# Optimization experiments

Measured on AMD Instinct MI355X. Metric: run time of the kernel, lower is better.

## Reference

```python
import jax, jax.numpy as jnp
import numpy as np

HEAD_DIM = 128

def setup_inputs() -> dict:
    key = jax.random.key(0)
    k1, k2, k3 = jax.random.split(key, 3)
    B, S, H, Hkv, D = 2, 2048, 32, 8, HEAD_DIM
    q = jax.random.normal(k1, (B, S, H, D), dtype=jnp.float32)
    k = jax.random.normal(k2, (B, S, Hkv, D), dtype=jnp.float32)
    v = jax.random.normal(k3, (B, S, Hkv, D), dtype=jnp.float32)
    return {"q": q, "k": k, "v": v}

def reference(q, k, v):
    # Causal GQA attention, same math as SDPA(is_causal=True, scale=head_dim**-0.5)
    # q: [B,S,H,D], k/v: [B,S,Hkv,D]; H = Hkv * G (grouped-query attention)
    B, S, H, D = q.shape
    Hkv = k.shape[2]
    G = H // Hkv
    scale = jnp.asarray(D, q.dtype) ** -0.5
    qg = q.reshape(B, S, Hkv, G, D)
    # scores: [B, Hkv, G, Sq, Sk]
    scores = jnp.einsum('bqhgd,bkhd->bhgqk', qg, k) * scale
    causal = jnp.tril(jnp.ones((S, S), dtype=bool))  # [Sq, Sk]
    scores = jnp.where(causal, scores, jnp.asarray(-jnp.inf, scores.dtype))
    probs = jax.nn.softmax(scores, axis=-1)
    out = jnp.einsum('bhgqk,bkhd->bqhgd', probs, v)
    return out.reshape(B, S, H, D)
```

## Files before the change

### kernel.cpp

```cpp
#include <hip/hip_runtime.h>
#include <hip/hip_bf16.h>

typedef short bf16x8 __attribute__((ext_vector_type(8)));
typedef float f32x4  __attribute__((ext_vector_type(4)));

#define B_    2
#define S_    2048
#define H_    32
#define HKV_  8
#define D_    128
#define QBLK  64
#define QBLK2 128
#define KVB   32
#define SCALE 0.1275431741f

static __device__ inline float exp2_fast(float x) {
    return __builtin_amdgcn_exp2f(x);
}

static __device__ inline unsigned short f2bf(float f) {
    unsigned u = __builtin_bit_cast(unsigned, f);
    u += 0x7fffu + ((u >> 16) & 1u);
    return (unsigned short)(u >> 16);
}
static __device__ inline unsigned pk2(float a, float b) {
    return (unsigned)f2bf(a) | ((unsigned)f2bf(b) << 16);
}
static __device__ inline short cvt_bf(float f) {
    __hip_bfloat16 h = __float2bfloat16(f);
    return __builtin_bit_cast(short, h);
}
static __device__ inline void gload16(const unsigned char* g, unsigned char* l) {
    __builtin_amdgcn_global_load_lds(
        (const __attribute__((address_space(1))) void*)g,
        (__attribute__((address_space(3))) void*)l, 16, 0, 0);
}

__global__ __launch_bounds__(256) void prep_k(const float* __restrict__ Kg,
                                              unsigned char* __restrict__ Kb) {
    const int s   = blockIdx.x * 256 + threadIdx.x;
    const int seg = s & 15;
    const int kv  = (s >> 4) & (S_ - 1);
    const int bhk = s >> 15;
    const int hk  = bhk & (HKV_ - 1);
    const int b   = bhk >> 3;
    const float* src = Kg + ((size_t)(b * S_ + kv) * HKV_ + hk) * D_ + seg * 8;
    float4 x0 = *(const float4*)(src);
    float4 x1 = *(const float4*)(src + 4);
    uint4 u = { pk2(x0.x, x0.y), pk2(x0.z, x0.w), pk2(x1.x, x1.y), pk2(x1.z, x1.w) };
    *(uint4*)(Kb + ((size_t)(b * HKV_ + hk) * S_ + kv) * 256 + ((seg * 16) ^ ((kv & 7) << 4))) = u;
}

__global__ __launch_bounds__(256) void prep_v(const float* __restrict__ Vg,
                                              unsigned short* __restrict__ Vb) {
    const int blk  = blockIdx.x;
    const int half = blk & 1;
    const int tile = (blk >> 1) & 63;
    const int hk   = (blk >> 7) & (HKV_ - 1);
    const int b    = blk >> 10;
    const int t    = threadIdx.x;
    const int kp0  = (t & 3) * 8;
    const int d    = (t >> 2) + half * 64;
    const int kv0  = tile * KVB;
    unsigned short tmp[8];
#pragma unroll
    for (int j = 0; j < 8; ++j) {
        const int kp = kp0 + j;
        const int kv = (((kp >> 2) & 1) << 4) + ((kp >> 3) << 2) + (kp & 3);
        tmp[j] = f2bf(Vg[((size_t)(b * S_ + kv0 + kv) * HKV_ + hk) * D_ + d]);
    }
    unsigned short* dst = Vb + ((size_t)(b * HKV_ + hk) * 64 + tile) * (128 * 32) + d * 32 + kp0;
    *(uint4*)dst = *(uint4*)tmp;
}

__global__ __launch_bounds__(256) void fattn2(
        const float* __restrict__ Qg, const unsigned char* __restrict__ Kb,
        const unsigned char* __restrict__ Vb, float* __restrict__ Og) {
    __shared__ __align__(16) unsigned char lds[2 * 16384];

    const int tid  = threadIdx.x;
    const int lane = tid & 63;
    const int w    = tid >> 6;
    const int m    = lane & 15;
    const int g    = lane >> 4;
    const int lane16 = lane * 16;

    const int SQ  = S_ / QBLK2;
    const int bid = blockIdx.x;
    const int qt  = (SQ - 1) - (bid >> 6);
    const int hb  = bid & 63;
    const int h   = hb & (H_ - 1);
    const int b   = hb >> 5;
    const int hk  = h >> 2;

    const int qB    = qt * QBLK2;
    const int q0w   = qB + w * 32;
    const int qA    = q0w + m;
    const int qgate = q0w + 31;

    const unsigned char* KbH = Kb + (size_t)(b * HKV_ + hk) * S_ * 256;
    const unsigned char* VbH = Vb + (size_t)(b * HKV_ + hk) * 64 * 8192;

    bf16x8 qfA[4], qfB[4];
    {
        const float* qrowA = Qg + (size_t)((b * S_ + qA) * H_ + h) * D_;
        const float* qrowB = qrowA + (size_t)16 * H_ * D_;
#pragma unroll
        for (int db = 0; db < 4; ++db) {
            const float* pA = qrowA + db * 32 + g * 8;
            const float* pB = qrowB + db * 32 + g * 8;
            float4 a0 = *(const float4*)(pA);
            float4 a1 = *(const float4*)(pA + 4);
            float4 b0 = *(const float4*)(pB);
            float4 b1 = *(const float4*)(pB + 4);
            bf16x8 qa, qb;
            qa[0] = cvt_bf(a0.x * SCALE); qa[1] = cvt_bf(a0.y * SCALE);
            qa[2] = cvt_bf(a0.z * SCALE); qa[3] = cvt_bf(a0.w * SCALE);
            qa[4] = cvt_bf(a1.x * SCALE); qa[5] = cvt_bf(a1.y * SCALE);
            qa[6] = cvt_bf(a1.z * SCALE); qa[7] = cvt_bf(a1.w * SCALE);
            qb[0] = cvt_bf(b0.x * SCALE); qb[1] = cvt_bf(b0.y * SCALE);
            qb[2] = cvt_bf(b0.z * SCALE); qb[3] = cvt_bf(b0.w * SCALE);
            qb[4] = cvt_bf(b1.x * SCALE); qb[5] = cvt_bf(b1.y * SCALE);
            qb[6] = cvt_bf(b1.z * SCALE); qb[7] = cvt_bf(b1.w * SCALE);
            qfA[db] = qa; qfB[db] = qb;
        }
    }

    f32x4 oaccA[8], oaccB[8];
#pragma unroll
    for (int i = 0; i < 8; ++i) {
        oaccA[i] = (f32x4){0.f, 0.f, 0.f, 0.f};
        oaccB[i] = (f32x4){0.f, 0.f, 0.f, 0.f};
    }
    float m_run = 4.0f, lsumA = 0.f, lsumB = 0.f;

#define STAGE(kt, cbuf) do {                                                  \
        const unsigned char* KbT = KbH + (size_t)(kt) * (KVB * 256);          \
        const unsigned char* VbT = VbH + (size_t)(kt) * 8192;                 \
        unsigned char* dK = lds + (cbuf) * 16384;                             \
        unsigned char* dV = dK + 8192;                                        \
        gload16(KbT + (w * 2 + 0) * 1024 + lane16, dK + (w * 2 + 0) * 1024);  \
        gload16(KbT + (w * 2 + 1) * 1024 + lane16, dK + (w * 2 + 1) * 1024);  \
        gload16(VbT + (w * 2 + 0) * 1024 + lane16, dV + (w * 2 + 0) * 1024);  \
        gload16(VbT + (w * 2 + 1) * 1024 + lane16, dV + (w * 2 + 1) * 1024);  \
    } while (0)

    const int nt = (qB + QBLK2) / KVB;
    int cur = 0;
    STAGE(0, 0);
    asm volatile("s_waitcnt vmcnt(0)" ::: "memory");
    __builtin_amdgcn_s_barrier();

    for (int t = 0; t < nt; ++t) {
        const int kv0 = t * KVB;
        if (t + 1 < nt) STAGE(t + 1, cur ^ 1);

        if (kv0 <= qgate) {
            const unsigned char* cK = lds + cur * 16384;
            const unsigned char* cV = cK + 8192;

            const f32x4 cinit = (f32x4){-m_run, -m_run, -m_run, -m_run};
            f32x4 stA0 = cinit, stA1 = cinit, stB0 = cinit, stB1 = cinit;
            const int sw = (m & 7) << 4;
            __builtin_amdgcn_s_setprio(1);
#pragma unroll
            for (int db = 0; db < 4; ++db) {
                bf16x8 kf0 = *(const bf16x8*)(cK + (m     ) * 256 + ((db * 64 + g * 16) ^ sw));
                bf16x8 kf1 = *(const bf16x8*)(cK + (m + 16) * 256 + ((db * 64 + g * 16) ^ sw));
                stA0 = __builtin_amdgcn_mfma_f32_16x16x32_bf16(kf0, qfA[db], stA0, 0, 0, 0);
                stA1 = __builtin_amdgcn_mfma_f32_16x16x32_bf16(kf1, qfA[db], stA1, 0, 0, 0);
                stB0 = __builtin_amdgcn_mfma_f32_16x16x32_bf16(kf0, qfB[db], stB0, 0, 0, 0);
                stB1 = __builtin_amdgcn_mfma_f32_16x16x32_bf16(kf1, qfB[db], stB1, 0, 0, 0);
            }
            __builtin_amdgcn_s_setprio(0);

            if (kv0 + (KVB - 1) > q0w) {
                const int qBrow = qA + 16;
#pragma unroll
                for (int jj = 0; jj < 4; ++jj) {
                    const int kva = kv0 + g * 4 + jj;
                    if (kva      > qA)    stA0[jj] = -1e30f;
                    if (kva + 16 > qA)    stA1[jj] = -1e30f;
                    if (kva      > qBrow) stB0[jj] = -1e30f;
                    if (kva + 16 > qBrow) stB1[jj] = -1e30f;
                }
            }

            float pmax = -1e30f;
#pragma unroll
            for (int jj = 0; jj < 4; ++jj)
                pmax = fmaxf(pmax, fmaxf(fmaxf(stA0[jj], stA1[jj]),
                                         fmaxf(stB0[jj], stB1[jj])));
            if (__any(pmax > 12.0f)) {
                float dm = fmaxf(pmax, __shfl_xor(pmax, 16));
                dm = fmaxf(dm, __shfl_xor(dm, 32));
                dm = fmaxf(dm, 0.0f);
                const float corr = exp2_fast(-dm);
                lsumA *= corr; lsumB *= corr;
                float cj[4];
#pragma unroll
                for (int jj = 0; jj < 4; ++jj) cj[jj] = __shfl(corr, g * 4 + jj);
#pragma unroll
                for (int i = 0; i < 8; ++i)
#pragma unroll
                    for (int jj = 0; jj < 4; ++jj) {
                        oaccA[i][jj] *= cj[jj];
                        oaccB[i][jj] *= cj[jj];
                    }
                m_run += dm;
#pragma unroll
                for (int jj = 0; jj < 4; ++jj) {
                    stA0[jj] -= dm; stA1[jj] -= dm;
                    stB0[jj] -= dm; stB1[jj] -= dm;
                }
            }

#pragma unroll
            for (int jj = 0; jj < 4; ++jj) {
                stA0[jj] = exp2_fast(stA0[jj]);
                stA1[jj] = exp2_fast(stA1[jj]);
                stB0[jj] = exp2_fast(stB0[jj]);
                stB1[jj] = exp2_fast(stB1[jj]);
            }
            lsumA += ((stA0[0] + stA0[1]) + (stA0[2] + stA0[3]))
                   + ((stA1[0] + stA1[1]) + (stA1[2] + stA1[3]));
            lsumB += ((stB0[0] + stB0[1]) + (stB0[2] + stB0[3]))
                   + ((stB1[0] + stB1[1]) + (stB1[2] + stB1[3]));

            bf16x8 paA, paB;
#pragma unroll
            for (int jj = 0; jj < 4; ++jj) {
                paA[jj]     = cvt_bf(stA0[jj]);
                paA[4 + jj] = cvt_bf(stA1[jj]);
                paB[jj]     = cvt_bf(stB0[jj]);
                paB[4 + jj] = cvt_bf(stB1[jj]);
            }

            __builtin_amdgcn_s_setprio(1);
#pragma unroll
            for (int db8 = 0; db8 < 8; ++db8) {
                bf16x8 vf = *(const bf16x8*)(cV + (db8 * 16 + m) * 64 + g * 16);
                oaccA[db8] = __builtin_amdgcn_mfma_f32_16x16x32_bf16(paA, vf, oaccA[db8], 0, 0, 0);
                oaccB[db8] = __builtin_amdgcn_mfma_f32_16x16x32_bf16(paB, vf, oaccB[db8], 0, 0, 0);
            }
            __builtin_amdgcn_s_setprio(0);
        }

        asm volatile("s_waitcnt vmcnt(0)" ::: "memory");
        __builtin_amdgcn_s_barrier();
        cur ^= 1;
    }
#undef STAGE

    lsumA += __shfl_xor(lsumA, 16); lsumA += __shfl_xor(lsumA, 32);
    lsumB += __shfl_xor(lsumB, 16); lsumB += __shfl_xor(lsumB, 32);
    const float rA = 1.0f / lsumA, rB = 1.0f / lsumB;
    float rsA[4], rsB[4];
#pragma unroll
    for (int jj = 0; jj < 4; ++jj) {
        rsA[jj] = __shfl(rA, g * 4 + jj);
        rsB[jj] = __shfl(rB, g * 4 + jj);
    }
#pragma unroll
    for (int db8 = 0; db8 < 8; ++db8) {
#pragma unroll
        for (int jj = 0; jj < 4; ++jj) {
            const int qrA = q0w + g * 4 + jj;
            Og[(size_t)((b * S_ + qrA) * H_ + h) * D_ + db8 * 16 + m]
                = oaccA[db8][jj] * rsA[jj];
            Og[(size_t)((b * S_ + qrA + 16) * H_ + h) * D_ + db8 * 16 + m]
                = oaccB[db8][jj] * rsB[jj];
        }
    }
}

__global__ __launch_bounds__(256) void fattn_fallback(
        const float* __restrict__ Qg, const float* __restrict__ Kg,
        const float* __restrict__ Vg, float* __restrict__ Og) {
    __shared__ __align__(16) unsigned char  sK[32 * 256];
    __shared__ __align__(16) unsigned short sV[128 * 40];
    const int tid  = threadIdx.x;
    const int lane = tid & 63;
    const int w    = tid >> 6;
    const int m    = lane & 15;
    const int g    = lane >> 4;
    const int SQ = S_ / QBLK;
    const int bid = blockIdx.x;
    const int qt  = bid % SQ;
    const int h   = (bid / SQ) % H_;
    const int b   = bid / (SQ * H_);
    const int hk  = h >> 2;
    const int qB    = qt * QBLK;
    const int q0w   = qB + w * 16;
    const int q_abs = q0w + m;
    const float SC = 0.08838834764831845f;
    bf16x8 qf[4];
    {
        const float* qrow = Qg + (size_t)((b * S_ + q_abs) * H_ + h) * D_;
#pragma unroll
        for (int db = 0; db < 4; ++db) {
            const float* p = qrow + db * 32 + g * 8;
            float4 a = *(const float4*)(p);
            float4 c = *(const float4*)(p + 4);
            bf16x8 q8;
            q8[0] = (short)f2bf(a.x * SC); q8[1] = (short)f2bf(a.y * SC);
            q8[2] = (short)f2bf(a.z * SC); q8[3] = (short)f2bf(a.w * SC);
            q8[4] = (short)f2bf(c.x * SC); q8[5] = (short)f2bf(c.y * SC);
            q8[6] = (short)f2bf(c.z * SC); q8[7] = (short)f2bf(c.w * SC);
            qf[db] = q8;
        }
    }
    f32x4 oacc[8];
#pragma unroll
    for (int i = 0; i < 8; ++i) oacc[i] = (f32x4){0.f, 0.f, 0.f, 0.f};
    float m_run = -1e30f, lsum = 0.f;
    const int nt = (qB + QBLK) / KVB;
    for (int t = 0; t < nt; ++t) {
        const int kv0 = t * KVB;
        __syncthreads();
        {
            const int r = tid >> 3, seg = tid & 7;
            const float* src = Kg + (size_t)((b * S_ + kv0 + r) * HKV_ + hk) * D_ + seg * 16;
            float4 x0 = *(const float4*)(src + 0);
            float4 x1 = *(const float4*)(src + 4);
            float4 x2 = *(const float4*)(src + 8);
            float4 x3 = *(const float4*)(src + 12);
            uint4 u0 = { pk2(x0.x,x0.y), pk2(x0.z,x0.w), pk2(x1.x,x1.y), pk2(x1.z,x1.w) };
            uint4 u1 = { pk2(x2.x,x2.y), pk2(x2.z,x2.w), pk2(x3.x,x3.y), pk2(x3.z,x3.w) };
            const int colb = seg * 32;
            const int sw   = (r & 7) << 4;
            *(uint4*)(sK + r * 256 + ((colb     ) ^ sw)) = u0;
            *(uint4*)(sK + r * 256 + ((colb + 16) ^ sw)) = u1;
        }
        {
            const int kv = tid & 31, d0 = (tid >> 5) * 16;
            const int kp = (((kv & 15) >> 2) << 3) + ((kv >> 4) << 2) + (kv & 3);
            const float* src = Vg + (size_t)((b * S_ + kv0 + kv) * HKV_ + hk) * D_ + d0;
#pragma unroll
            for (int i = 0; i < 4; ++i) {
                float4 x = *(const float4*)(src + i * 4);
                const int d = d0 + i * 4;
                sV[(d + 0) * 40 + kp] = f2bf(x.x);
                sV[(d + 1) * 40 + kp] = f2bf(x.y);
                sV[(d + 2) * 40 + kp] = f2bf(x.z);
                sV[(d + 3) * 40 + kp] = f2bf(x.w);
            }
        }
        __syncthreads();
        if (kv0 > q0w + 15) continue;
        f32x4 st0 = (f32x4){0.f,0.f,0.f,0.f}, st1 = st0;
#pragma unroll
        for (int db = 0; db < 4; ++db) {
            const int sw = (m & 7) << 4;
            bf16x8 kf0 = *(const bf16x8*)(sK + (m      ) * 256 + ((db * 64 + g * 16) ^ sw));
            bf16x8 kf1 = *(const bf16x8*)(sK + (m + 16 ) * 256 + ((db * 64 + g * 16) ^ sw));
            st0 = __builtin_amdgcn_mfma_f32_16x16x32_bf16(kf0, qf[db], st0, 0, 0, 0);
            st1 = __builtin_amdgcn_mfma_f32_16x16x32_bf16(kf1, qf[db], st1, 0, 0, 0);
        }
        float p[8];
        float tm = -1e30f;
#pragma unroll
        for (int jj = 0; jj < 4; ++jj) {
            int kva = kv0 + g * 4 + jj;
            float s0 = (kva       <= q_abs) ? st0[jj] : -1e30f;
            float s1 = (kva + 16  <= q_abs) ? st1[jj] : -1e30f;
            p[jj]     = s0;
            p[4 + jj] = s1;
            tm = fmaxf(tm, fmaxf(s0, s1));
        }
        tm = fmaxf(tm, __shfl_xor(tm, 16));
        tm = fmaxf(tm, __shfl_xor(tm, 32));
        const float m_new = fmaxf(m_run, tm);
        const float corr  = __expf(m_run - m_new);
        float ls = 0.f;
#pragma unroll
        for (int i = 0; i < 8; ++i) { float e = __expf(p[i] - m_new); p[i] = e; ls += e; }
        ls += __shfl_xor(ls, 16);
        ls += __shfl_xor(ls, 32);
        lsum  = lsum * corr + ls;
        m_run = m_new;
        float cj[4];
#pragma unroll
        for (int jj = 0; jj < 4; ++jj) cj[jj] = __shfl(corr, g * 4 + jj);
#pragma unroll
        for (int i = 0; i < 8; ++i)
#pragma unroll
            for (int jj = 0; jj < 4; ++jj) oacc[i][jj] *= cj[jj];
        bf16x8 pa;
#pragma unroll
        for (int i = 0; i < 8; ++i) pa[i] = (short)f2bf(p[i]);
#pragma unroll
        for (int db8 = 0; db8 < 8; ++db8) {
            bf16x8 vf = *(const bf16x8*)((const unsigned char*)sV +
                          (((db8 * 16 + m) * 40 + g * 8) * 2));
            oacc[db8] = __builtin_amdgcn_mfma_f32_16x16x32_bf16(pa, vf, oacc[db8], 0, 0, 0);
        }
    }
    float rs[4];
    const float rinv = 1.0f / lsum;
#pragma unroll
    for (int jj = 0; jj < 4; ++jj) rs[jj] = __shfl(rinv, g * 4 + jj);
#pragma unroll
    for (int db8 = 0; db8 < 8; ++db8) {
#pragma unroll
        for (int jj = 0; jj < 4; ++jj) {
            const int qr = q0w + g * 4 + jj;
            Og[(size_t)((b * S_ + qr) * H_ + h) * D_ + db8 * 16 + m] = oacc[db8][jj] * rs[jj];
        }
    }
}

extern "C" void kernel_launch(void* const* d_in, const int* in_sizes, int n_in,
                              void* d_out, int out_size, void* d_ws, size_t ws_size,
                              hipStream_t stream) {
    const float* q = (const float*)d_in[0];
    const float* k = (const float*)d_in[1];
    const float* v = (const float*)d_in[2];
    float* o = (float*)d_out;

    const size_t KB_BYTES = (size_t)B_ * HKV_ * S_ * 256;
    const size_t VB_BYTES = (size_t)B_ * HKV_ * 64 * 128 * 32 * 2;

    if (ws_size >= KB_BYTES + VB_BYTES) {
        unsigned char*  Kb = (unsigned char*)d_ws;
        unsigned short* Vb = (unsigned short*)((unsigned char*)d_ws + KB_BYTES);
        prep_k<<<2048, 256, 0, stream>>>(k, Kb);
        prep_v<<<2048, 256, 0, stream>>>(v, Vb);
        const int blocks = B_ * H_ * (S_ / QBLK2);
        fattn2<<<blocks, 256, 0, stream>>>(q, Kb, (const unsigned char*)Vb, o);
    } else {
        const int blocks = B_ * H_ * (S_ / QBLK);
        fattn_fallback<<<blocks, 256, 0, stream>>>(q, k, v, o);
    }
}
```

Baseline: 124.2 us.

## Pair causal query tiles per block and triple-buffer K/V staging

```diff
diff --git a/kernel.cpp b/kernel.cpp
--- a/kernel.cpp
+++ b/kernel.cpp
@@ -73,10 +73,10 @@
     *(uint4*)dst = *(uint4*)tmp;
 }
 
-__global__ __launch_bounds__(256) void fattn2(
+__global__ __launch_bounds__(256) void fattn6(
         const float* __restrict__ Qg, const unsigned char* __restrict__ Kb,
         const unsigned char* __restrict__ Vb, float* __restrict__ Og) {
-    __shared__ __align__(16) unsigned char lds[2 * 16384];
+    __shared__ __align__(16) unsigned char lds[3 * 16384];
 
     const int tid  = threadIdx.x;
     const int lane = tid & 63;
@@ -84,58 +84,21 @@
     const int m    = lane & 15;
     const int g    = lane >> 4;
     const int lane16 = lane * 16;
-
-    const int SQ  = S_ / QBLK2;
-    const int bid = blockIdx.x;
-    const int qt  = (SQ - 1) - (bid >> 6);
-    const int hb  = bid & 63;
-    const int h   = hb & (H_ - 1);
-    const int b   = hb >> 5;
-    const int hk  = h >> 2;
-
-    const int qB    = qt * QBLK2;
-    const int q0w   = qB + w * 32;
-    const int qA    = q0w + m;
-    const int qgate = q0w + 31;
+    const int sw   = (m & 7) << 4;
+
+    const int bid  = blockIdx.x;
+    const int pair = bid >> 6;
+    const int hb   = bid & 63;
+    const int h    = hb & (H_ - 1);
+    const int b    = hb >> 5;
+    const int hk   = h >> 2;
 
     const unsigned char* KbH = Kb + (size_t)(b * HKV_ + hk) * S_ * 256;
     const unsigned char* VbH = Vb + (size_t)(b * HKV_ + hk) * 64 * 8192;
-
-    bf16x8 qfA[4], qfB[4];
-    {
-        const float* qrowA = Qg + (size_t)((b * S_ + qA) * H_ + h) * D_;
-        const float* qrowB = qrowA + (size_t)16 * H_ * D_;
-#pragma unroll
-        for (int db = 0; db < 4; ++db) {
-            const float* pA = qrowA + db * 32 + g * 8;
-            const float* pB = qrowB + db * 32 + g * 8;
-            float4 a0 = *(const float4*)(pA);
-            float4 a1 = *(const float4*)(pA + 4);
-            float4 b0 = *(const float4*)(pB);
-            float4 b1 = *(const float4*)(pB + 4);
-            bf16x8 qa, qb;
-            qa[0] = cvt_bf(a0.x * SCALE); qa[1] = cvt_bf(a0.y * SCALE);
-            qa[2] = cvt_bf(a0.z * SCALE); qa[3] = cvt_bf(a0.w * SCALE);
-            qa[4] = cvt_bf(a1.x * SCALE); qa[5] = cvt_bf(a1.y * SCALE);
-            qa[6] = cvt_bf(a1.z * SCALE); qa[7] = cvt_bf(a1.w * SCALE);
-            qb[0] = cvt_bf(b0.x * SCALE); qb[1] = cvt_bf(b0.y * SCALE);
-            qb[2] = cvt_bf(b0.z * SCALE); qb[3] = cvt_bf(b0.w * SCALE);
-            qb[4] = cvt_bf(b1.x * SCALE); qb[5] = cvt_bf(b1.y * SCALE);
-            qb[6] = cvt_bf(b1.z * SCALE); qb[7] = cvt_bf(b1.w * SCALE);
-            qfA[db] = qa; qfB[db] = qb;
-        }
-    }
-
-    f32x4 oaccA[8], oaccB[8];
-#pragma unroll
-    for (int i = 0; i < 8; ++i) {
-        oaccA[i] = (f32x4){0.f, 0.f, 0.f, 0.f};
-        oaccB[i] = (f32x4){0.f, 0.f, 0.f, 0.f};
-    }
-    float m_run = 4.0f, lsumA = 0.f, lsumB = 0.f;
+    const float* QgH = Qg + (size_t)(b * S_ * H_ + h) * D_;
 
 #define STAGE(kt, cbuf) do {                                                  \
-        const unsigned char* KbT = KbH + (size_t)(kt) * (KVB * 256);          \
+        const unsigned char* KbT = KbH + (size_t)(kt) * 8192;                 \
         const unsigned char* VbT = VbH + (size_t)(kt) * 8192;                 \
         unsigned char* dK = lds + (cbuf) * 16384;                             \
         unsigned char* dV = dK + 8192;                                        \
@@ -145,133 +108,183 @@
         gload16(VbT + (w * 2 + 1) * 1024 + lane16, dV + (w * 2 + 1) * 1024);  \
     } while (0)
 
-    const int nt = (qB + QBLK2) / KVB;
-    int cur = 0;
-    STAGE(0, 0);
-    asm volatile("s_waitcnt vmcnt(0)" ::: "memory");
-    __builtin_amdgcn_s_barrier();
-
-    for (int t = 0; t < nt; ++t) {
-        const int kv0 = t * KVB;
-        if (t + 1 < nt) STAGE(t + 1, cur ^ 1);
-
-        if (kv0 <= qgate) {
-            const unsigned char* cK = lds + cur * 16384;
-            const unsigned char* cV = cK + 8192;
-
-            const f32x4 cinit = (f32x4){-m_run, -m_run, -m_run, -m_run};
-            f32x4 stA0 = cinit, stA1 = cinit, stB0 = cinit, stB1 = cinit;
-            const int sw = (m & 7) << 4;
-            __builtin_amdgcn_s_setprio(1);
+    for (int job = 0; job < 2; ++job) {
+        const int qt    = (job == 0) ? (15 - pair) : pair;
+        const int qB    = qt * QBLK2;
+        const int q0w   = qB + w * 32;
+        const int qA    = q0w + m;
+        const int qgate = q0w + 31;
+
+        bf16x8 qfA[4], qfB[4];
+        {
+            const float* qrowA = QgH + (size_t)qA * H_ * D_;
+            const float* qrowB = qrowA + (size_t)16 * H_ * D_;
 #pragma unroll
             for (int db = 0; db < 4; ++db) {
-                bf16x8 kf0 = *(const bf16x8*)(cK + (m     ) * 256 + ((db * 64 + g * 16) ^ sw));
-                bf16x8 kf1 = *(const bf16x8*)(cK + (m + 16) * 256 + ((db * 64 + g * 16) ^ sw));
-                stA0 = __builtin_amdgcn_mfma_f32_16x16x32_bf16(kf0, qfA[db], stA0, 0, 0, 0);
-                stA1 = __builtin_amdgcn_mfma_f32_16x16x32_bf16(kf1, qfA[db], stA1, 0, 0, 0);
-                stB0 = __builtin_amdgcn_mfma_f32_16x16x32_bf16(kf0, qfB[db], stB0, 0, 0, 0);
-                stB1 = __builtin_amdgcn_mfma_f32_16x16x32_bf16(kf1, qfB[db], stB1, 0, 0, 0);
+                const float* pA = qrowA + db * 32 + g * 8;
+                const float* pB = qrowB + db * 32 + g * 8;
+                float4 a0 = *(const float4*)(pA);
+                float4 a1 = *(const float4*)(pA + 4);
+                float4 b0 = *(const float4*)(pB);
+                float4 b1 = *(const float4*)(pB + 4);
+                bf16x8 qa, qb;
+                qa[0] = cvt_bf(a0.x * SCALE); qa[1] = cvt_bf(a0.y * SCALE);
+                qa[2] = cvt_bf(a0.z * SCALE); qa[3] = cvt_bf(a0.w * SCALE);
+                qa[4] = cvt_bf(a1.x * SCALE); qa[5] = cvt_bf(a1.y * SCALE);
+                qa[6] = cvt_bf(a1.z * SCALE); qa[7] = cvt_bf(a1.w * SCALE);
+                qb[0] = cvt_bf(b0.x * SCALE); qb[1] = cvt_bf(b0.y * SCALE);
+                qb[2] = cvt_bf(b0.z * SCALE); qb[3] = cvt_bf(b0.w * SCALE);
+                qb[4] = cvt_bf(b1.x * SCALE); qb[5] = cvt_bf(b1.y * SCALE);
+                qb[6] = cvt_bf(b1.z * SCALE); qb[7] = cvt_bf(b1.w * SCALE);
+                qfA[db] = qa; qfB[db] = qb;
             }
-            __builtin_amdgcn_s_setprio(0);
-
-            if (kv0 + (KVB - 1) > q0w) {
-                const int qBrow = qA + 16;
+        }
+
+        f32x4 oaccA[8], oaccB[8];
+#pragma unroll
+        for (int i = 0; i < 8; ++i) {
+            oaccA[i] = (f32x4){0.f, 0.f, 0.f, 0.f};
+            oaccB[i] = (f32x4){0.f, 0.f, 0.f, 0.f};
+        }
+        float m_run = 4.0f, lsumA = 0.f, lsumB = 0.f;
+
+        const int nt = 4 * (qt + 1);
+        STAGE(0, 0);
+        STAGE(1, 1);
+        int bc = 0;
+        int bs = 2;
+
+        for (int t = 0; t < nt; ++t) {
+            const int kv0 = t * KVB;
+
+            if (t + 1 < nt) asm volatile("s_waitcnt vmcnt(4)" ::: "memory");
+            else            asm volatile("s_waitcnt vmcnt(0)" ::: "memory");
+            __builtin_amdgcn_s_barrier();
+
+            if (t + 2 < nt) {
+                STAGE(t + 2, bs);
+                bs = (bs + 1 == 3) ? 0 : bs + 1;
+            }
+
+            if (kv0 <= qgate) {
+                const unsigned char* cK = lds + bc * 16384;
+                const unsigned char* cV = cK + 8192;
+
+                const f32x4 cinit = (f32x4){-m_run, -m_run, -m_run, -m_run};
+                f32x4 stA0 = cinit, stA1 = cinit, stB0 = cinit, stB1 = cinit;
+                __builtin_amdgcn_s_setprio(1);
+#pragma unroll
+                for (int db = 0; db < 4; ++db) {
+                    const int co = (db * 64 + g * 16) ^ sw;
+                    bf16x8 kf0 = *(const bf16x8*)(cK + (m     ) * 256 + co);
+                    bf16x8 kf1 = *(const bf16x8*)(cK + (m + 16) * 256 + co);
+                    stA0 = __builtin_amdgcn_mfma_f32_16x16x32_bf16(kf0, qfA[db], stA0, 0, 0, 0);
+                    stA1 = __builtin_amdgcn_mfma_f32_16x16x32_bf16(kf1, qfA[db], stA1, 0, 0, 0);
+                    stB0 = __builtin_amdgcn_mfma_f32_16x16x32_bf16(kf0, qfB[db], stB0, 0, 0, 0);
+                    stB1 = __builtin_amdgcn_mfma_f32_16x16x32_bf16(kf1, qfB[db], stB1, 0, 0, 0);
+                }
+                __builtin_amdgcn_s_setprio(0);
+
+                if (kv0 + (KVB - 1) > q0w) {
+                    const int qBrow = qA + 16;
+#pragma unroll
+                    for (int jj = 0; jj < 4; ++jj) {
+                        const int kva = kv0 + g * 4 + jj;
+                        if (kva      > qA)    stA0[jj] = -1e30f;
+                        if (kva + 16 > qA)    stA1[jj] = -1e30f;
+                        if (kva      > qBrow) stB0[jj] = -1e30f;
+                        if (kva + 16 > qBrow) stB1[jj] = -1e30f;
+                    }
+                }
+
+                float pmax = -1e30f;
+#pragma unroll
+                for (int jj = 0; jj < 4; ++jj)
+                    pmax = fmaxf(pmax, fmaxf(fmaxf(stA0[jj], stA1[jj]),
+                                             fmaxf(stB0[jj], stB1[jj])));
+                if (__any(pmax > 12.0f)) {
+                    float dm = fmaxf(pmax, __shfl_xor(pmax, 16));
+                    dm = fmaxf(dm, __shfl_xor(dm, 32));
+                    dm = fmaxf(dm, 0.0f);
+                    const float corr = exp2_fast(-dm);
+                    lsumA *= corr; lsumB *= corr;
+                    float cj[4];
+#pragma unroll
+                    for (int jj = 0; jj < 4; ++jj) cj[jj] = __shfl(corr, g * 4 + jj);
+#pragma unroll
+                    for (int i = 0; i < 8; ++i)
+#pragma unroll
+                        for (int jj = 0; jj < 4; ++jj) {
+                            oaccA[i][jj] *= cj[jj];
+                            oaccB[i][jj] *= cj[jj];
+                        }
+                    m_run += dm;
+#pragma unroll
+                    for (int jj = 0; jj < 4; ++jj) {
+                        stA0[jj] -= dm; stA1[jj] -= dm;
+                        stB0[jj] -= dm; stB1[jj] -= dm;
+                    }
+                }
+
 #pragma unroll
                 for (int jj = 0; jj < 4; ++jj) {
-                    const int kva = kv0 + g * 4 + jj;
-                    if (kva      > qA)    stA0[jj] = -1e30f;
-                    if (kva + 16 > qA)    stA1[jj] = -1e30f;
-                    if (kva      > qBrow) stB0[jj] = -1e30f;
-                    if (kva + 16 > qBrow) stB1[jj] = -1e30f;
-                }
+                    stA0[jj] = exp2_fast(stA0[jj]);
+                    stA1[jj] = exp2_fast(stA1[jj]);
+                    stB0[jj] = exp2_fast(stB0[jj]);
+                    stB1[jj] = exp2_fast(stB1[jj]);
+                }
+                lsumA += ((stA0[0] + stA0[1]) + (stA0[2] + stA0[3]))
+                       + ((stA1[0] + stA1[1]) + (stA1[2] + stA1[3]));
+                lsumB += ((stB0[0] + stB0[1]) + (stB0[2] + stB0[3]))
+                       + ((stB1[0] + stB1[1]) + (stB1[2] + stB1[3]));
+
+                bf16x8 paA, paB;
+#pragma unroll
+                for (int jj = 0; jj < 4; ++jj) {
+                    paA[jj]     = cvt_bf(stA0[jj]);
+                    paA[4 + jj] = cvt_bf(stA1[jj]);
+                    paB[jj]     = cvt_bf(stB0[jj]);
+                    paB[4 + jj] = cvt_bf(stB1[jj]);
+                }
+
+                __builtin_amdgcn_s_setprio(1);
+#pragma unroll
+                for (int db8 = 0; db8 < 8; ++db8) {
+                    bf16x8 vf = *(const bf16x8*)(cV + (db8 * 16 + m) * 64 + g * 16);
+                    oaccA[db8] = __builtin_amdgcn_mfma_f32_16x16x32_bf16(paA, vf, oaccA[db8], 0, 0, 0);
+                    oaccB[db8] = __builtin_amdgcn_mfma_f32_16x16x32_bf16(paB, vf, oaccB[db8], 0, 0, 0);
+                }
+                __builtin_amdgcn_s_setprio(0);
             }
 
-            float pmax = -1e30f;
-#pragma unroll
-            for (int jj = 0; jj < 4; ++jj)
-                pmax = fmaxf(pmax, fmaxf(fmaxf(stA0[jj], stA1[jj]),
-                                         fmaxf(stB0[jj], stB1[jj])));
-            if (__any(pmax > 12.0f)) {
-                float dm = fmaxf(pmax, __shfl_xor(pmax, 16));
-                dm = fmaxf(dm, __shfl_xor(dm, 32));
-                dm = fmaxf(dm, 0.0f);
-                const float corr = exp2_fast(-dm);
-                lsumA *= corr; lsumB *= corr;
-                float cj[4];
-#pragma unroll
-                for (int jj = 0; jj < 4; ++jj) cj[jj] = __shfl(corr, g * 4 + jj);
-#pragma unroll
-                for (int i = 0; i < 8; ++i)
-#pragma unroll
-                    for (int jj = 0; jj < 4; ++jj) {
-                        oaccA[i][jj] *= cj[jj];
-                        oaccB[i][jj] *= cj[jj];
-                    }
-                m_run += dm;
-#pragma unroll
-                for (int jj = 0; jj < 4; ++jj) {
-                    stA0[jj] -= dm; stA1[jj] -= dm;
-                    stB0[jj] -= dm; stB1[jj] -= dm;
-                }
+            bc = (bc + 1 == 3) ? 0 : bc + 1;
+        }
+
+        lsumA += __shfl_xor(lsumA, 16); lsumA += __shfl_xor(lsumA, 32);
+        lsumB += __shfl_xor(lsumB, 16); lsumB += __shfl_xor(lsumB, 32);
+        const float rA = 1.0f / lsumA, rB = 1.0f / lsumB;
+        float rsA[4], rsB[4];
+#pragma unroll
+        for (int jj = 0; jj < 4; ++jj) {
+            rsA[jj] = __shfl(rA, g * 4 + jj);
+            rsB[jj] = __shfl(rB, g * 4 + jj);
+        }
+#pragma unroll
+        for (int db8 = 0; db8 < 8; ++db8) {
+#pragma unroll
+            for (int jj = 0; jj < 4; ++jj) {
+                const int qrA = q0w + g * 4 + jj;
+                Og[(size_t)((b * S_ + qrA) * H_ + h) * D_ + db8 * 16 + m]
+                    = oaccA[db8][jj] * rsA[jj];
+                Og[(size_t)((b * S_ + qrA + 16) * H_ + h) * D_ + db8 * 16 + m]
+                    = oaccB[db8][jj] * rsB[jj];
             }
-
-#pragma unroll
-            for (int jj = 0; jj < 4; ++jj) {
-                stA0[jj] = exp2_fast(stA0[jj]);
-                stA1[jj] = exp2_fast(stA1[jj]);
-                stB0[jj] = exp2_fast(stB0[jj]);
-                stB1[jj] = exp2_fast(stB1[jj]);
-            }
-            lsumA += ((stA0[0] + stA0[1]) + (stA0[2] + stA0[3]))
-                   + ((stA1[0] + stA1[1]) + (stA1[2] + stA1[3]));
-            lsumB += ((stB0[0] + stB0[1]) + (stB0[2] + stB0[3]))
-                   + ((stB1[0] + stB1[1]) + (stB1[2] + stB1[3]));
-
-            bf16x8 paA, paB;
-#pragma unroll
-            for (int jj = 0; jj < 4; ++jj) {
-                paA[jj]     = cvt_bf(stA0[jj]);
-                paA[4 + jj] = cvt_bf(stA1[jj]);
-                paB[jj]     = cvt_bf(stB0[jj]);
-                paB[4 + jj] = cvt_bf(stB1[jj]);
-            }
-
-            __builtin_amdgcn_s_setprio(1);
-#pragma unroll
-            for (int db8 = 0; db8 < 8; ++db8) {
-                bf16x8 vf = *(const bf16x8*)(cV + (db8 * 16 + m) * 64 + g * 16);
-                oaccA[db8] = __builtin_amdgcn_mfma_f32_16x16x32_bf16(paA, vf, oaccA[db8], 0, 0, 0);
-                oaccB[db8] = __builtin_amdgcn_mfma_f32_16x16x32_bf16(paB, vf, oaccB[db8], 0, 0, 0);
-            }
-            __builtin_amdgcn_s_setprio(0);
-        }
-
-        asm volatile("s_waitcnt vmcnt(0)" ::: "memory");
+        }
+
+        asm volatile("" ::: "memory");
         __builtin_amdgcn_s_barrier();
-        cur ^= 1;
     }
 #undef STAGE
-
-    lsumA += __shfl_xor(lsumA, 16); lsumA += __shfl_xor(lsumA, 32);
-    lsumB += __shfl_xor(lsumB, 16); lsumB += __shfl_xor(lsumB, 32);
-    const float rA = 1.0f / lsumA, rB = 1.0f / lsumB;
-    float rsA[4], rsB[4];
-#pragma unroll
-    for (int jj = 0; jj < 4; ++jj) {
-        rsA[jj] = __shfl(rA, g * 4 + jj);
-        rsB[jj] = __shfl(rB, g * 4 + jj);
-    }
-#pragma unroll
-    for (int db8 = 0; db8 < 8; ++db8) {
-#pragma unroll
-        for (int jj = 0; jj < 4; ++jj) {
-            const int qrA = q0w + g * 4 + jj;
-            Og[(size_t)((b * S_ + qrA) * H_ + h) * D_ + db8 * 16 + m]
-                = oaccA[db8][jj] * rsA[jj];
-            Og[(size_t)((b * S_ + qrA + 16) * H_ + h) * D_ + db8 * 16 + m]
-                = oaccB[db8][jj] * rsB[jj];
-        }
-    }
 }
 
 __global__ __launch_bounds__(256) void fattn_fallback(
@@ -314,9 +327,9 @@
 #pragma unroll
     for (int i = 0; i < 8; ++i) oacc[i] = (f32x4){0.f, 0.f, 0.f, 0.f};
     float m_run = -1e30f, lsum = 0.f;
-    const int nt = (qB + QBLK) / KVB;
+    const int nt = (qB + QBLK) / 32;
     for (int t = 0; t < nt; ++t) {
-        const int kv0 = t * KVB;
+        const int kv0 = t * 32;
         __syncthreads();
         {
             const int r = tid >> 3, seg = tid & 7;
@@ -328,9 +341,9 @@
             uint4 u0 = { pk2(x0.x,x0.y), pk2(x0.z,x0.w), pk2(x1.x,x1.y), pk2(x1.z,x1.w) };
             uint4 u1 = { pk2(x2.x,x2.y), pk2(x2.z,x2.w), pk2(x3.x,x3.y), pk2(x3.z,x3.w) };
             const int colb = seg * 32;
-            const int sw   = (r & 7) << 4;
-            *(uint4*)(sK + r * 256 + ((colb     ) ^ sw)) = u0;
-            *(uint4*)(sK + r * 256 + ((colb + 16) ^ sw)) = u1;
+            const int swz  = (r & 7) << 4;
+            *(uint4*)(sK + r * 256 + ((colb     ) ^ swz)) = u0;
+            *(uint4*)(sK + r * 256 + ((colb + 16) ^ swz)) = u1;
         }
         {
             const int kv = tid & 31, d0 = (tid >> 5) * 16;
@@ -351,9 +364,9 @@
         f32x4 st0 = (f32x4){0.f,0.f,0.f,0.f}, st1 = st0;
 #pragma unroll
         for (int db = 0; db < 4; ++db) {
-            const int sw = (m & 7) << 4;
-            bf16x8 kf0 = *(const bf16x8*)(sK + (m      ) * 256 + ((db * 64 + g * 16) ^ sw));
-            bf16x8 kf1 = *(const bf16x8*)(sK + (m + 16 ) * 256 + ((db * 64 + g * 16) ^ sw));
+            const int swz = (m & 7) << 4;
+            bf16x8 kf0 = *(const bf16x8*)(sK + (m      ) * 256 + ((db * 64 + g * 16) ^ swz));
+            bf16x8 kf1 = *(const bf16x8*)(sK + (m + 16 ) * 256 + ((db * 64 + g * 16) ^ swz));
             st0 = __builtin_amdgcn_mfma_f32_16x16x32_bf16(kf0, qf[db], st0, 0, 0, 0);
             st1 = __builtin_amdgcn_mfma_f32_16x16x32_bf16(kf1, qf[db], st1, 0, 0, 0);
         }
@@ -426,8 +439,7 @@
         unsigned short* Vb = (unsigned short*)((unsigned char*)d_ws + KB_BYTES);
         prep_k<<<2048, 256, 0, stream>>>(k, Kb);
         prep_v<<<2048, 256, 0, stream>>>(v, Vb);
-        const int blocks = B_ * H_ * (S_ / QBLK2);
-        fattn2<<<blocks, 256, 0, stream>>>(q, Kb, (const unsigned char*)Vb, o);
+        fattn6<<<512, 256, 0, stream>>>(q, Kb, (const unsigned char*)Vb, o);
     } else {
         const int blocks = B_ * H_ * (S_ / QBLK);
         fattn_fallback<<<blocks, 256, 0, stream>>>(q, k, v, o);
```

New measurement: 137.0 us. 1.1x slower.
